# Kernel tuning notes

Measured on AMD Instinct MI355X. Metric: run time of the kernel, lower is better.

The kernel has to match this reference:

```python
import jax, jax.numpy as jnp
import numpy as np


def setup_inputs() -> dict:
    key = jax.random.key(0)
    k1, k2 = jax.random.split(key)
    B, OUT_DIM, S = 4, 1024, 2048
    IN_DIM = 4096
    x = jax.random.normal(k1, (B, OUT_DIM, S), dtype=jnp.float32)
    w = jax.random.normal(k2, (IN_DIM, OUT_DIM), dtype=jnp.float32) * 0.02
    return {"x": x, "w": w}


def reference(x, w):
    # Original: mse[b,i,s] = mean_o (w[i,o] - x[b,o,s])^2
    # Computed via the squared-distance expansion to avoid the
    # (B, in_dim, S, out_dim) broadcast intermediate:
    #   mean_o (w-x)^2 = (||w||^2 - 2 w.x + ||x||^2) / out_dim
    out_dim = w.shape[1]
    w2 = jnp.sum(w * w, axis=1)[None, :, None]            # (1, in_dim, 1)
    x2 = jnp.sum(x * x, axis=1)[:, None, :]               # (B, 1, S)
    wx = jnp.einsum('io,bos->bis', w, x)                  # (B, in_dim, S)
    return (w2 - 2.0 * wx + x2) / out_dim
```

## Files before the change

kernel.cpp:

```cpp
#include <hip/hip_runtime.h>
#include <stdint.h>


#define M_DIM 4096
#define K_DIM 1024
#define N_DIM 2048
#define B_DIM 4
#define NF 8192

#define BM 256
#define BN 256
#define NKT 4
#define MT (M_DIM / BM)
#define NT (NF / BN)
#define BUFB 65536

typedef __attribute__((ext_vector_type(4))) int i32x4;
typedef __attribute__((ext_vector_type(8))) int i32x8;
typedef __attribute__((ext_vector_type(4))) float f32x4;
typedef __attribute__((ext_vector_type(4))) float f32x4v;

__device__ __forceinline__ uint32_t fp4q(float a) {
  uint32_t s = (__float_as_uint(a) >> 31) << 3;
  float t = fabsf(a);
  int idx = (t > 0.25f) + (t > 0.75f) + (t > 1.25f) + (t > 1.75f) +
            (t > 2.5f) + (t > 3.5f) + (t > 5.0f);
  return s | (uint32_t)idx;
}

__global__ __launch_bounds__(256) void prep_all(const float* __restrict__ w,
                                                const float* __restrict__ x,
                                                uint8_t* __restrict__ w4,
                                                uint8_t* __restrict__ x4,
                                                float* __restrict__ w2,
                                                float* __restrict__ x2) {
  __shared__ uint8_t tile[64][68];
  __shared__ float red[4];
  const int bid = blockIdx.x;
  const int t = threadIdx.x;

  if (bid < M_DIM) {
    const int i = bid;
    f32x4v v =
        __builtin_nontemporal_load(((const f32x4v*)(w + (size_t)i * K_DIM)) + t);
    float ss = v.x * v.x + v.y * v.y + v.z * v.z + v.w * v.w;
    ushort pk = (ushort)(fp4q(v.x * 64.0f) | (fp4q(v.y * 64.0f) << 4) |
                         (fp4q(v.z * 64.0f) << 8) | (fp4q(v.w * 64.0f) << 12));
    ((ushort*)(w4 + (size_t)i * 512))[t] = pk;
#pragma unroll
    for (int off = 32; off > 0; off >>= 1) ss += __shfl_down(ss, off);
    if ((t & 63) == 0) red[t >> 6] = ss;
    __syncthreads();
    if (t == 0) w2[i] = red[0] + red[1] + red[2] + red[3];
    return;
  }

  const int idx = bid - M_DIM;
  const int s0 = (idx & 31) * 64;
  const int o0 = ((idx >> 5) & 15) * 64;
  const int b = idx >> 9;
  const int tr = t >> 4;
  const int tc = t & 15;
  float ss0 = 0, ss1 = 0, ss2 = 0, ss3 = 0;
#pragma unroll
  for (int p = 0; p < 4; ++p) {
    const int r = p * 16 + tr;
    f32x4v v = __builtin_nontemporal_load(
        ((const f32x4v*)(x + ((size_t)(b * K_DIM + o0 + r)) * N_DIM + s0)) + tc);
    ss0 += v.x * v.x; ss1 += v.y * v.y; ss2 += v.z * v.z; ss3 += v.w * v.w;
    tile[r][tc * 4 + 0] = (uint8_t)fp4q(v.x);
    tile[r][tc * 4 + 1] = (uint8_t)fp4q(v.y);
    tile[r][tc * 4 + 2] = (uint8_t)fp4q(v.z);
    tile[r][tc * 4 + 3] = (uint8_t)fp4q(v.w);
  }
  ss0 += __shfl_xor(ss0, 16); ss0 += __shfl_xor(ss0, 32);
  ss1 += __shfl_xor(ss1, 16); ss1 += __shfl_xor(ss1, 32);
  ss2 += __shfl_xor(ss2, 16); ss2 += __shfl_xor(ss2, 32);
  ss3 += __shfl_xor(ss3, 16); ss3 += __shfl_xor(ss3, 32);
  if ((t & 63) < 16) {
    float* xp = x2 + b * N_DIM + s0 + tc * 4;
    atomicAdd(xp + 0, ss0);
    atomicAdd(xp + 1, ss1);
    atomicAdd(xp + 2, ss2);
    atomicAdd(xp + 3, ss3);
  }
  __syncthreads();
#pragma unroll
  for (int p = 0; p < 4; ++p) {
    const int s = p * 16 + tr;
    const int sF = b * N_DIM + s0 + s;
    const int a = tc * 4;
    ushort bb = (ushort)(tile[a][s] | (tile[a + 1][s] << 4) |
                         (tile[a + 2][s] << 8) | (tile[a + 3][s] << 12));
    ((ushort*)(x4 + (size_t)sF * 512 + (o0 >> 1)))[tc] = bb;
  }
}

typedef const __attribute__((address_space(1))) uint32_t* gp_t;
typedef __attribute__((address_space(3))) uint32_t* lp_t;

__device__ __forceinline__ void gload_lds16(const void* g, const void* l) {
  __builtin_amdgcn_global_load_lds((gp_t)(uintptr_t)g,
                                   (lp_t)(uint32_t)(uintptr_t)l, 16, 0, 0);
}

__device__ __forceinline__ f32x4 mfma4(i32x4 a, i32x4 b, f32x4 c) {
  i32x8 a8 = {a[0], a[1], a[2], a[3], 0, 0, 0, 0};
  i32x8 b8 = {b[0], b[1], b[2], b[3], 0, 0, 0, 0};
  return __builtin_amdgcn_mfma_scale_f32_16x16x128_f8f6f4(a8, b8, c, 4, 4, 0,
                                                          127, 0, 127);
}
#define FENCE() asm volatile("" ::: "memory")

__global__ __launch_bounds__(512) void gemm_mse4(
    const uint8_t* __restrict__ w4, const uint8_t* __restrict__ x4,
    const float* __restrict__ w2, const float* __restrict__ x2,
    float* __restrict__ out) {
  __shared__ __align__(32) char smem[2 * BUFB];
  const int tid = threadIdx.x;
  const int wid = tid >> 6;
  const int lane = tid & 63;
  const int laneR = lane & 15;
  const int g = lane >> 4;
  const int wm = wid >> 2;
  const int wn = wid & 3;

  const int bid = blockIdx.x;
  const int xcd = bid & 7;
  const int r = bid >> 3;
  const int st = r >> 4;
  const int sub = r & 15;
  const int mt = st * 4 + (sub & 3);
  const int nt = xcd * 4 + (sub >> 2);

  const uint8_t* Ag = w4 + (size_t)mt * BM * 512;
  const uint8_t* Bg = x4 + (size_t)nt * BN * 512;

#define SRCOFF(P) ((size_t)((P) >> 7) * 512 + (((P) ^ ((((P) >> 7) & 7) << 4)) & 127))
  const int p0 = tid * 16;
  const uint8_t* sA0 = Ag + SRCOFF(p0);
  const uint8_t* sA1 = Ag + SRCOFF(p0 + 8192);
  const uint8_t* sA2 = Ag + SRCOFF(p0 + 16384);
  const uint8_t* sA3 = Ag + SRCOFF(p0 + 24576);
  const uint8_t* sB0 = Bg + SRCOFF(p0);
  const uint8_t* sB1 = Bg + SRCOFF(p0 + 8192);
  const uint8_t* sB2 = Bg + SRCOFF(p0 + 16384);
  const uint8_t* sB3 = Bg + SRCOFF(p0 + 24576);

#define STAGE(tt, buf)                                   \
  {                                                      \
    const int ko_ = (tt) * 128;                          \
    char* lb_ = smem + (buf) * BUFB;                     \
    gload_lds16(sA0 + ko_, lb_ + p0);                    \
    gload_lds16(sA1 + ko_, lb_ + p0 + 8192);             \
    gload_lds16(sA2 + ko_, lb_ + p0 + 16384);            \
    gload_lds16(sA3 + ko_, lb_ + p0 + 24576);            \
    gload_lds16(sB0 + ko_, lb_ + 32768 + p0);            \
    gload_lds16(sB1 + ko_, lb_ + 32768 + p0 + 8192);     \
    gload_lds16(sB2 + ko_, lb_ + 32768 + p0 + 16384);    \
    gload_lds16(sB3 + ko_, lb_ + 32768 + p0 + 24576);    \
  }

  const int swz = (laneR & 7) << 4;
  const int t0 = (g << 4) ^ swz;
  const int t1 = (64 | (g << 4)) ^ swz;
  const int offA_ = (wm * 128 + laneR) * 128;
  const int offB_ = 32768 + (wn * 64 + laneR) * 128;

#define LDF4(off, bo) (*(const i32x4*)(smem + (bo) + (off)))

  f32x4 acc[8][4] = {};

  STAGE(0, 0);
  asm volatile("s_waitcnt vmcnt(0)" ::: "memory");
  __builtin_amdgcn_s_barrier();
  FENCE();

#pragma unroll
  for (int t = 0; t < NKT; ++t) {
    const int bo = (t & 1) * BUFB;
    if (t < NKT - 1) STAGE(t + 1, (t + 1) & 1);
    i32x4 b00 = LDF4(offB_ + 0 * 2048 + t0, bo);
    i32x4 b10 = LDF4(offB_ + 1 * 2048 + t0, bo);
    i32x4 b20 = LDF4(offB_ + 2 * 2048 + t0, bo);
    i32x4 b30 = LDF4(offB_ + 3 * 2048 + t0, bo);
    i32x4 b01 = LDF4(offB_ + 0 * 2048 + t1, bo);
    i32x4 b11 = LDF4(offB_ + 1 * 2048 + t1, bo);
    i32x4 b21 = LDF4(offB_ + 2 * 2048 + t1, bo);
    i32x4 b31 = LDF4(offB_ + 3 * 2048 + t1, bo);
    __builtin_amdgcn_s_setprio(1);
#pragma unroll
    for (int mi = 0; mi < 8; ++mi) {
      i32x4 a0 = LDF4(offA_ + mi * 2048 + t0, bo);
      acc[mi][0] = mfma4(a0, b00, acc[mi][0]);
      acc[mi][1] = mfma4(a0, b10, acc[mi][1]);
      acc[mi][2] = mfma4(a0, b20, acc[mi][2]);
      acc[mi][3] = mfma4(a0, b30, acc[mi][3]);
      i32x4 a1 = LDF4(offA_ + mi * 2048 + t1, bo);
      acc[mi][0] = mfma4(a1, b01, acc[mi][0]);
      acc[mi][1] = mfma4(a1, b11, acc[mi][1]);
      acc[mi][2] = mfma4(a1, b21, acc[mi][2]);
      acc[mi][3] = mfma4(a1, b31, acc[mi][3]);
    }
    __builtin_amdgcn_s_setprio(0);
    asm volatile("s_waitcnt vmcnt(0)" ::: "memory");
    asm volatile("s_waitcnt lgkmcnt(0)" ::: "memory");
    __builtin_amdgcn_sched_barrier(0);
    __builtin_amdgcn_s_barrier();
    FENCE();
  }

  const float cA = 0.03125f;
  const float inv = 1.0f / (float)K_DIM;
  const int rowb0 = mt * BM + wm * 128;
  const int colf0 = nt * BN + wn * 64;
  const int bz = colf0 >> 11;
  const int sc0 = colf0 & (N_DIM - 1);
  float xv[4];
#pragma unroll
  for (int ni = 0; ni < 4; ++ni) xv[ni] = x2[colf0 + ni * 16 + laneR];
  float* lds_f = (float*)smem + wid * 4096;
  float* outp = out + (size_t)bz * M_DIM * N_DIM;

#pragma unroll
  for (int miH = 0; miH < 2; ++miH) {
#pragma unroll
    for (int mi4 = 0; mi4 < 4; ++mi4) {
      const int mi = miH * 4 + mi4;
#pragma unroll
      for (int j = 0; j < 4; ++j) {
        const int r2 = mi4 * 16 + g * 4 + j;
        const float wv = w2[rowb0 + miH * 64 + r2];
#pragma unroll
        for (int ni = 0; ni < 4; ++ni) {
          const int c = ni * 16 + laneR;
          lds_f[r2 * 64 + (c ^ ((r2 & 7) << 2))] =
              (wv + xv[ni] - acc[mi][ni][j] * cA) * inv;
        }
      }
    }
#pragma unroll
    for (int k = 0; k < 16; ++k) {
      const int r2 = k * 4 + (lane >> 4);
      const int c0 = laneR * 4;
      f32x4 v = *(const f32x4*)&lds_f[r2 * 64 + (c0 ^ ((r2 & 7) << 2))];
      *(f32x4*)(outp + (size_t)(rowb0 + miH * 64 + r2) * N_DIM + sc0 + c0) = v;
    }
    asm volatile("s_waitcnt lgkmcnt(0)" ::: "memory");
  }
#undef STAGE
#undef LDF4
#undef SRCOFF
}

extern "C" void kernel_launch(void* const* d_in, const int* in_sizes, int n_in,
                              void* d_out, int out_size, void* d_ws, size_t ws_size,
                              hipStream_t stream) {
  const float* x = (const float*)d_in[0];
  const float* w = (const float*)d_in[1];
  float* out = (float*)d_out;
  char* ws = (char*)d_ws;
  uint8_t* w4 = (uint8_t*)ws;
  uint8_t* x4 = (uint8_t*)(ws + (size_t)(2 << 20));
  float* w2 = (float*)(ws + (size_t)(8 << 20));
  float* x2 = w2 + M_DIM;

  (void)hipMemsetAsync(x2, 0, NF * sizeof(float), stream);
  prep_all<<<dim3(M_DIM + 2048), dim3(256), 0, stream>>>(w, x, w4, x4, w2, x2);
  gemm_mse4<<<dim3(MT * NT), dim3(512), 0, stream>>>(w4, x4, w2, x2, out);
}
```

Baseline: 71.40 us.

## Restructure prep so each block reduces full columns, dropping memset and global atomics

The prep kernel now uses 512-thread blocks. Each w block quantizes two rows, and each x block covers all 1024 input channels for 32 sequence positions. Because the x block sees every channel, it finishes the squared-norm reduction in shared memory and writes x2 directly, so the hipMemsetAsync launch and the global atomicAdds go away. The trade-offs are a larger shared tile (about 33KB), strided byte stores into shared memory that may hit bank conflicts, and fewer, heavier blocks with less coalesced packed-output writes.

```diff
diff --git a/kernel.cpp b/kernel.cpp
--- a/kernel.cpp
+++ b/kernel.cpp
@@ -28,71 +28,71 @@
   return s | (uint32_t)idx;
 }
 
-__global__ __launch_bounds__(256) void prep_all(const float* __restrict__ w,
+__global__ __launch_bounds__(512) void prep_all(const float* __restrict__ w,
                                                 const float* __restrict__ x,
                                                 uint8_t* __restrict__ w4,
                                                 uint8_t* __restrict__ x4,
                                                 float* __restrict__ w2,
                                                 float* __restrict__ x2) {
-  __shared__ uint8_t tile[64][68];
-  __shared__ float red[4];
+  __shared__ uint8_t tile[32][1028];
+  __shared__ float xacc[32];
+  __shared__ float red[8];
   const int bid = blockIdx.x;
   const int t = threadIdx.x;
 
-  if (bid < M_DIM) {
-    const int i = bid;
+  if (bid < 2048) {
+    const int i = bid * 2 + (t >> 8);
+    const int tt = t & 255;
     f32x4v v =
-        __builtin_nontemporal_load(((const f32x4v*)(w + (size_t)i * K_DIM)) + t);
+        __builtin_nontemporal_load(((const f32x4v*)(w + (size_t)i * K_DIM)) + tt);
     float ss = v.x * v.x + v.y * v.y + v.z * v.z + v.w * v.w;
     ushort pk = (ushort)(fp4q(v.x * 64.0f) | (fp4q(v.y * 64.0f) << 4) |
                          (fp4q(v.z * 64.0f) << 8) | (fp4q(v.w * 64.0f) << 12));
-    ((ushort*)(w4 + (size_t)i * 512))[t] = pk;
+    ((ushort*)(w4 + (size_t)i * 512))[tt] = pk;
 #pragma unroll
     for (int off = 32; off > 0; off >>= 1) ss += __shfl_down(ss, off);
     if ((t & 63) == 0) red[t >> 6] = ss;
     __syncthreads();
     if (t == 0) w2[i] = red[0] + red[1] + red[2] + red[3];
+    if (t == 256) w2[i] = red[4] + red[5] + red[6] + red[7];
     return;
   }
 
-  const int idx = bid - M_DIM;
-  const int s0 = (idx & 31) * 64;
-  const int o0 = ((idx >> 5) & 15) * 64;
-  const int b = idx >> 9;
-  const int tr = t >> 4;
-  const int tc = t & 15;
-  float ss0 = 0, ss1 = 0, ss2 = 0, ss3 = 0;
-#pragma unroll
-  for (int p = 0; p < 4; ++p) {
-    const int r = p * 16 + tr;
+  const int idx = bid - 2048;
+  const int s0 = (idx & 63) * 32;
+  const int b = idx >> 6;
+  const int tr = t >> 3;
+  const int tc = t & 7;
+  if (t < 32) xacc[t] = 0.0f;
+  float p0 = 0, p1 = 0, p2 = 0, p3 = 0;
+#pragma unroll
+  for (int p = 0; p < 16; ++p) {
+    const int o = p * 64 + tr;
     f32x4v v = __builtin_nontemporal_load(
-        ((const f32x4v*)(x + ((size_t)(b * K_DIM + o0 + r)) * N_DIM + s0)) + tc);
-    ss0 += v.x * v.x; ss1 += v.y * v.y; ss2 += v.z * v.z; ss3 += v.w * v.w;
-    tile[r][tc * 4 + 0] = (uint8_t)fp4q(v.x);
-    tile[r][tc * 4 + 1] = (uint8_t)fp4q(v.y);
-    tile[r][tc * 4 + 2] = (uint8_t)fp4q(v.z);
-    tile[r][tc * 4 + 3] = (uint8_t)fp4q(v.w);
-  }
-  ss0 += __shfl_xor(ss0, 16); ss0 += __shfl_xor(ss0, 32);
-  ss1 += __shfl_xor(ss1, 16); ss1 += __shfl_xor(ss1, 32);
-  ss2 += __shfl_xor(ss2, 16); ss2 += __shfl_xor(ss2, 32);
-  ss3 += __shfl_xor(ss3, 16); ss3 += __shfl_xor(ss3, 32);
-  if ((t & 63) < 16) {
-    float* xp = x2 + b * N_DIM + s0 + tc * 4;
-    atomicAdd(xp + 0, ss0);
-    atomicAdd(xp + 1, ss1);
-    atomicAdd(xp + 2, ss2);
-    atomicAdd(xp + 3, ss3);
+        (const f32x4v*)(x + ((size_t)(b * K_DIM + o)) * N_DIM + s0 + tc * 4));
+    p0 += v.x * v.x; p1 += v.y * v.y; p2 += v.z * v.z; p3 += v.w * v.w;
+    tile[tc * 4 + 0][o] = (uint8_t)fp4q(v.x);
+    tile[tc * 4 + 1][o] = (uint8_t)fp4q(v.y);
+    tile[tc * 4 + 2][o] = (uint8_t)fp4q(v.z);
+    tile[tc * 4 + 3][o] = (uint8_t)fp4q(v.w);
   }
   __syncthreads();
-#pragma unroll
-  for (int p = 0; p < 4; ++p) {
-    const int s = p * 16 + tr;
-    const int sF = b * N_DIM + s0 + s;
-    const int a = tc * 4;
-    ushort bb = (ushort)(tile[a][s] | (tile[a + 1][s] << 4) |
-                         (tile[a + 2][s] << 8) | (tile[a + 3][s] << 12));
-    ((ushort*)(x4 + (size_t)sF * 512 + (o0 >> 1)))[tc] = bb;
+  atomicAdd(&xacc[tc * 4 + 0], p0);
+  atomicAdd(&xacc[tc * 4 + 1], p1);
+  atomicAdd(&xacc[tc * 4 + 2], p2);
+  atomicAdd(&xacc[tc * 4 + 3], p3);
+  __syncthreads();
+  if (t < 32) x2[b * N_DIM + s0 + t] = xacc[t];
+  {
+    const int s = t >> 4;
+    const int u0 = (t & 15) * 16;
+    ushort* orow = (ushort*)(x4 + ((size_t)(b * N_DIM + s0 + s)) * 512);
+#pragma unroll
+    for (int u = 0; u < 16; ++u) {
+      const int a = (u0 + u) * 4;
+      orow[u0 + u] = (ushort)(tile[s][a] | (tile[s][a + 1] << 4) |
+                              (tile[s][a + 2] << 8) | (tile[s][a + 3] << 12));
+    }
   }
 }
 
@@ -265,7 +265,6 @@
   float* w2 = (float*)(ws + (size_t)(8 << 20));
   float* x2 = w2 + M_DIM;
 
-  (void)hipMemsetAsync(x2, 0, NF * sizeof(float), stream);
-  prep_all<<<dim3(M_DIM + 2048), dim3(256), 0, stream>>>(w, x, w4, x4, w2, x2);
+  prep_all<<<dim3(2048 + 256), dim3(512), 0, stream>>>(w, x, w4, x4, w2, x2);
   gemm_mse4<<<dim3(MT * NT), dim3(512), 0, stream>>>(w4, x4, w2, x2, out);
 }
```

New measurement: 65.52 us (median of 2 runs). 8.2% less time.
